# Performance work log

Hardware: AMD Instinct MI355X
Metric: run time of the kernel (lower is better)

## Reference

```python
import jax, jax.numpy as jnp
import numpy as np

NUM_HEADS = 16


def _bayes_w(mu, rho, eps):
    # reparameterized weight sample: w = mu + softplus(rho) * eps
    return mu + jax.nn.softplus(rho) * eps


def setup_inputs() -> dict:
    key = jax.random.key(0)
    ks = jax.random.split(key, 12)
    B, N, C = 4, 2048, 1024
    x = jax.random.normal(ks[0], (B, N, C), jnp.float32)
    w_scale = 0.02
    q_w = jax.random.normal(ks[1], (C, C), jnp.float32) * w_scale
    k_w = jax.random.normal(ks[2], (C, C), jnp.float32) * w_scale
    v_mu = jax.random.normal(ks[3], (C, C), jnp.float32) * w_scale
    v_rho = jax.random.normal(ks[4], (C, C), jnp.float32) * 0.1 - 3.0
    v_eps = jax.random.normal(ks[5], (C, C), jnp.float32)
    proj_mu = jax.random.normal(ks[6], (C, C), jnp.float32) * w_scale
    proj_rho = jax.random.normal(ks[7], (C, C), jnp.float32) * 0.1 - 3.0
    proj_eps = jax.random.normal(ks[8], (C, C), jnp.float32)
    pb_mu = jax.random.normal(ks[9], (C,), jnp.float32) * w_scale
    pb_rho = jax.random.normal(ks[10], (C,), jnp.float32) * 0.1 - 3.0
    pb_eps = jax.random.normal(ks[11], (C,), jnp.float32)
    return {"x": x, "q_w": q_w, "k_w": k_w, "v_mu": v_mu, "v_rho": v_rho,
            "v_eps": v_eps, "proj_mu": proj_mu, "proj_rho": proj_rho,
            "proj_eps": proj_eps, "pb_mu": pb_mu, "pb_rho": pb_rho,
            "pb_eps": pb_eps}


def reference(x, q_w, k_w, v_mu, v_rho, v_eps, proj_mu, proj_rho, proj_eps,
              pb_mu, pb_rho, pb_eps):
    B, N, C = x.shape
    H = NUM_HEADS
    D = C // H
    scale = D ** -0.5
    v_w = _bayes_w(v_mu, v_rho, v_eps)
    # projections (torch Linear: y = x @ W.T)
    q = (x @ q_w.T).reshape(B, N, H, D).transpose(0, 2, 1, 3)  # [B,H,N,D]
    k = (x @ k_w.T).reshape(B, N, H, D).transpose(0, 2, 1, 3)
    v = (x @ v_w.T).reshape(B, N, H, D).transpose(0, 2, 1, 3)
    attn = jax.nn.softmax(jnp.einsum("bhnd,bhmd->bhnm", q * scale, k), axis=-1)
    out = jnp.einsum("bhnm,bhmd->bhnd", attn, v)
    out = out.transpose(0, 2, 1, 3).reshape(B, N, C)
    p_w = _bayes_w(proj_mu, proj_rho, proj_eps)
    p_b = _bayes_w(pb_mu, pb_rho, pb_eps)
    return out @ p_w.T + p_b
```

## Files before the change

### kernel.cpp

```cpp
#include <hip/hip_runtime.h>
#include <hip/hip_bf16.h>
#include <cstdint>
#include <math.h>

typedef __bf16 bf16;
typedef __bf16 bf16x8 __attribute__((ext_vector_type(8)));
typedef __bf16 bf16x4 __attribute__((ext_vector_type(4)));
typedef float  f32x4 __attribute__((ext_vector_type(4)));

#define LOG2E 1.4426950408889634f

#if __has_builtin(__builtin_amdgcn_exp2f)
#define EXP2(x) __builtin_amdgcn_exp2f(x)
#else
#define EXP2(x) exp2f(x)
#endif

#define AS1 __attribute__((address_space(1)))
#define AS3 __attribute__((address_space(3)))

__device__ __forceinline__ void gload_lds16(const bf16* g, bf16* l) {
    __builtin_amdgcn_global_load_lds((AS1 void*)g, (AS3 void*)l, 16, 0, 0);
}

__global__ __launch_bounds__(256)
void cast_f32_bf16(const float* __restrict__ in, bf16* __restrict__ out, int n4) {
    int i = blockIdx.x * 256 + threadIdx.x;
    if (i < n4) {
        float4 v = ((const float4*)in)[i];
        bf16 o[4] = {(bf16)v.x, (bf16)v.y, (bf16)v.z, (bf16)v.w};
        *(uint64_t*)&((bf16*)out)[i * 4] = *(uint64_t*)o;
    }
}

__global__ __launch_bounds__(256)
void bayes_w_kernel(const float* __restrict__ mu, const float* __restrict__ rho,
                    const float* __restrict__ eps, bf16* __restrict__ out, int n) {
    int i = blockIdx.x * 256 + threadIdx.x;
    if (i < n) {
        float r = rho[i];
        float sp = (r > 15.f) ? r : log1pf(expf(r));
        out[i] = (bf16)(mu[i] + sp * eps[i]);
    }
}

__global__ __launch_bounds__(256)
void bayes_b_kernel(const float* __restrict__ mu, const float* __restrict__ rho,
                    const float* __restrict__ eps, float* __restrict__ out, int n) {
    int i = blockIdx.x * 256 + threadIdx.x;
    if (i < n) {
        float r = rho[i];
        float sp = (r > 15.f) ? r : log1pf(expf(r));
        out[i] = mu[i] + sp * eps[i];
    }
}

template <typename OutT>
__global__ __launch_bounds__(256)
void gemm_bt(const bf16* __restrict__ A, const bf16* __restrict__ W,
             OutT* __restrict__ C, const float* __restrict__ bias,
             int M, int N, int K, float q_scale, int q_cols) {
    __shared__ bf16 lA[128 * 32];
    __shared__ bf16 lB[128 * 32];

    const int lane = threadIdx.x & 63;
    const int wv   = threadIdx.x >> 6;
    const int wr   = wv >> 1, wc = wv & 1;
    const int m0 = blockIdx.y * 128, n0 = blockIdx.x * 128;
    const int col = lane & 15, quad = lane >> 4;
    const float scale = (n0 < q_cols) ? q_scale : 1.0f;

    const int srow  = wv * 16 + (lane >> 2);
    const int skcol = (lane & 3) * 8;

    f32x4 acc[4][4] = {};

    for (int k0 = 0; k0 < K; k0 += 32) {
#pragma unroll
        for (int r = 0; r < 2; ++r) {
            gload_lds16(A + (size_t)(m0 + r * 64 + srow) * K + k0 + skcol,
                        &lA[(r * 64 + wv * 16) * 32]);
            gload_lds16(W + (size_t)(n0 + r * 64 + srow) * K + k0 + skcol,
                        &lB[(r * 64 + wv * 16) * 32]);
        }
        __syncthreads();

        bf16x8 af[4], bfr[4];
#pragma unroll
        for (int t = 0; t < 4; ++t) {
            af[t]  = *(const bf16x8*)&lA[(wr * 64 + t * 16 + col) * 32 + quad * 8];
            bfr[t] = *(const bf16x8*)&lB[(wc * 64 + t * 16 + col) * 32 + quad * 8];
        }
#pragma unroll
        for (int i = 0; i < 4; ++i)
#pragma unroll
            for (int j = 0; j < 4; ++j)
                acc[i][j] = __builtin_amdgcn_mfma_f32_16x16x32_bf16(af[i], bfr[j], acc[i][j], 0, 0, 0);
        __syncthreads();
    }

#pragma unroll
    for (int i = 0; i < 4; ++i) {
        int row = m0 + wr * 64 + i * 16 + quad * 4;
#pragma unroll
        for (int j = 0; j < 4; ++j) {
            int cc = n0 + wc * 64 + j * 16 + col;
            float bv = bias ? bias[cc] : 0.f;
#pragma unroll
            for (int r = 0; r < 4; ++r)
                C[(size_t)(row + r) * N + cc] = (OutT)(acc[i][j][r] * scale + bv);
        }
    }
}

__global__ __launch_bounds__(256, 4)
void attn_kernel(const bf16* __restrict__ QKV, bf16* __restrict__ O) {
    __shared__ bf16 sK [64 * 64];
    __shared__ bf16 sVt[64 * 72];
    __shared__ bf16 sP [128 * 72];

    const int lane = threadIdx.x & 63;
    const int wv   = threadIdx.x >> 6;
    const int col  = lane & 15, quad = lane >> 4;
    const int qt = blockIdx.x, h = blockIdx.y, b = blockIdx.z;

    const size_t rowQ0 = (size_t)b * 2048 + qt * 128;
    const bf16* Qg = QKV + rowQ0 * 3072 + h * 64;
    const bf16* Kg = QKV + (size_t)b * 2048 * 3072 + 1024 + h * 64;
    const bf16* Vg = QKV + (size_t)b * 2048 * 3072 + 2048 + h * 64;

#pragma unroll
    for (int it = 0; it < 4; ++it) {
        int c = it * 256 + threadIdx.x;
        int row = c >> 3, dc = (c & 7) * 8;
        *(bf16x8*)&sP[row * 72 + dc] = *(const bf16x8*)&Qg[(size_t)row * 3072 + dc];
    }
    __syncthreads();
    bf16x8 qf[2][2];
#pragma unroll
    for (int mi = 0; mi < 2; ++mi)
#pragma unroll
        for (int ks = 0; ks < 2; ++ks)
            qf[mi][ks] = *(const bf16x8*)&sP[(wv * 32 + mi * 16 + col) * 72 + ks * 32 + quad * 8];

    const int rloc = lane >> 3;
    const bf16* Kdma = Kg + (size_t)(wv * 16 + rloc) * 3072 + (((lane & 7) ^ rloc) * 8);

    f32x4 lsum[2] = {};
    f32x4 o[2][4] = {};
    const int cx = col & 7;

    for (int kv0 = 0; kv0 < 2048; kv0 += 64) {
        gload_lds16(Kdma + (size_t)kv0 * 3072,       &sK[(wv * 16) * 64]);
        gload_lds16(Kdma + (size_t)(kv0 + 8) * 3072, &sK[(wv * 16 + 8) * 64]);
#pragma unroll
        for (int it = 0; it < 2; ++it) {
            int c = it * 256 + threadIdx.x;
            int row = c & 63, dc = (c >> 6) * 8;
            bf16x8 v = *(const bf16x8*)&Vg[(size_t)(kv0 + row) * 3072 + dc];
#pragma unroll
            for (int j = 0; j < 8; ++j) sVt[(dc + j) * 72 + row] = v[j];
        }
        __syncthreads();

        f32x4 st[2][4];
#pragma unroll
        for (int nj = 0; nj < 4; ++nj) {
            bf16x8 kf0 = *(const bf16x8*)&sK[(nj * 16 + col) * 64 + ((quad ^ cx) * 8)];
            bf16x8 kf1 = *(const bf16x8*)&sK[(nj * 16 + col) * 64 + (((quad ^ cx) ^ 4) * 8)];
#pragma unroll
            for (int mi = 0; mi < 2; ++mi) {
                f32x4 t = {0.f, 0.f, 0.f, 0.f};
                t = __builtin_amdgcn_mfma_f32_16x16x32_bf16(kf0, qf[mi][0], t, 0, 0, 0);
                t = __builtin_amdgcn_mfma_f32_16x16x32_bf16(kf1, qf[mi][1], t, 0, 0, 0);
                st[mi][nj] = t;
            }
        }

#pragma unroll
        for (int mi = 0; mi < 2; ++mi) {
#pragma unroll
            for (int nj = 0; nj < 4; ++nj) {
                f32x4 p;
#pragma unroll
                for (int r = 0; r < 4; ++r) p[r] = EXP2(st[mi][nj][r]);
                lsum[mi] += p;
                bf16x4 pk = {(bf16)p[0], (bf16)p[1], (bf16)p[2], (bf16)p[3]};
                *(bf16x4*)&sP[(wv * 32 + mi * 16 + col) * 72 + nj * 16 + quad * 4] = pk;
            }
        }

#pragma unroll
        for (int ks = 0; ks < 2; ++ks) {
            bf16x8 pf0 = *(const bf16x8*)&sP[(wv * 32 + col) * 72 + ks * 32 + quad * 8];
            bf16x8 pf1 = *(const bf16x8*)&sP[(wv * 32 + 16 + col) * 72 + ks * 32 + quad * 8];
#pragma unroll
            for (int dj = 0; dj < 4; ++dj) {
                bf16x8 vf = *(const bf16x8*)&sVt[(dj * 16 + col) * 72 + ks * 32 + quad * 8];
                o[0][dj] = __builtin_amdgcn_mfma_f32_16x16x32_bf16(pf0, vf, o[0][dj], 0, 0, 0);
                o[1][dj] = __builtin_amdgcn_mfma_f32_16x16x32_bf16(pf1, vf, o[1][dj], 0, 0, 0);
            }
        }
        __syncthreads();
    }

#pragma unroll
    for (int mi = 0; mi < 2; ++mi) {
        float l = lsum[mi][0] + lsum[mi][1] + lsum[mi][2] + lsum[mi][3];
        l += __shfl_xor(l, 16, 64);
        l += __shfl_xor(l, 32, 64);
#pragma unroll
        for (int r = 0; r < 4; ++r) {
            float inv = 1.f / __shfl(l, quad * 4 + r, 64);
            size_t row = rowQ0 + wv * 32 + mi * 16 + quad * 4 + r;
#pragma unroll
            for (int dj = 0; dj < 4; ++dj)
                O[row * 1024 + h * 64 + dj * 16 + col] = (bf16)(o[mi][dj][r] * inv);
        }
    }
}

extern "C" void kernel_launch(void* const* d_in, const int* in_sizes, int n_in,
                              void* d_out, int out_size, void* d_ws, size_t ws_size,
                              hipStream_t stream) {
    const float* x      = (const float*)d_in[0];
    const float* q_w    = (const float*)d_in[1];
    const float* k_w    = (const float*)d_in[2];
    const float* v_mu   = (const float*)d_in[3];
    const float* v_rho  = (const float*)d_in[4];
    const float* v_eps  = (const float*)d_in[5];
    const float* p_mu   = (const float*)d_in[6];
    const float* p_rho  = (const float*)d_in[7];
    const float* p_eps  = (const float*)d_in[8];
    const float* pb_mu  = (const float*)d_in[9];
    const float* pb_rho = (const float*)d_in[10];
    const float* pb_eps = (const float*)d_in[11];
    float* out = (float*)d_out;

    const size_t MN = (size_t)8192 * 1024;
    const size_t MB = (size_t)1 << 20;
    char* ws = (char*)d_ws;
    bf16*  xb   = (bf16*)(ws);
    bf16*  wqkv = (bf16*)(ws + 16 * MB);
    bf16*  pwb  = (bf16*)(ws + 22 * MB);
    float* p_b  = (float*)(ws + 24 * MB);
    bf16*  QKV  = (bf16*)(ws + 25 * MB);
    bf16*  Ab   = xb;

    const int Wsz = 1024 * 1024;
    cast_f32_bf16<<<(int)(MN / 4 / 256), 256, 0, stream>>>(x, xb, (int)(MN / 4));
    cast_f32_bf16<<<1024, 256, 0, stream>>>(q_w, wqkv, Wsz / 4);
    cast_f32_bf16<<<1024, 256, 0, stream>>>(k_w, wqkv + Wsz, Wsz / 4);
    bayes_w_kernel<<<4096, 256, 0, stream>>>(v_mu, v_rho, v_eps, wqkv + 2 * Wsz, Wsz);
    bayes_w_kernel<<<4096, 256, 0, stream>>>(p_mu, p_rho, p_eps, pwb, Wsz);
    bayes_b_kernel<<<4, 256, 0, stream>>>(pb_mu, pb_rho, pb_eps, p_b, 1024);

    gemm_bt<bf16><<<dim3(24, 64), 256, 0, stream>>>(xb, wqkv, QKV, nullptr,
                                                    8192, 3072, 1024, 0.125f * LOG2E, 1024);

    attn_kernel<<<dim3(16, 16, 4), 256, 0, stream>>>(QKV, Ab);

    gemm_bt<float><<<dim3(8, 64), 256, 0, stream>>>(Ab, pwb, out, p_b,
                                                    8192, 1024, 1024, 1.0f, 1024);
}
```

Measured before the change: 342.8 us.

## Pre-transpose V, load K/V fragments directly from global, fuse prep kernels

```diff
diff --git a/kernel.cpp b/kernel.cpp
--- a/kernel.cpp
+++ b/kernel.cpp
@@ -7,20 +7,19 @@
 typedef __bf16 bf16x8 __attribute__((ext_vector_type(8)));
 typedef __bf16 bf16x4 __attribute__((ext_vector_type(4)));
 typedef float  f32x4 __attribute__((ext_vector_type(4)));
+typedef unsigned short u16x8 __attribute__((ext_vector_type(8)));
 
 #define LOG2E 1.4426950408889634f
-
-#if __has_builtin(__builtin_amdgcn_exp2f)
-#define EXP2(x) __builtin_amdgcn_exp2f(x)
-#else
-#define EXP2(x) exp2f(x)
-#endif
 
 #define AS1 __attribute__((address_space(1)))
 #define AS3 __attribute__((address_space(3)))
 
 __device__ __forceinline__ void gload_lds16(const bf16* g, bf16* l) {
     __builtin_amdgcn_global_load_lds((AS1 void*)g, (AS3 void*)l, 16, 0, 0);
+}
+
+__device__ __forceinline__ float softplus(float r) {
+    return (r > 15.f) ? r : log1pf(expf(r));
 }
 
 __global__ __launch_bounds__(256)
@@ -29,36 +28,63 @@
     if (i < n4) {
         float4 v = ((const float4*)in)[i];
         bf16 o[4] = {(bf16)v.x, (bf16)v.y, (bf16)v.z, (bf16)v.w};
-        *(uint64_t*)&((bf16*)out)[i * 4] = *(uint64_t*)o;
-    }
-}
-
-__global__ __launch_bounds__(256)
-void bayes_w_kernel(const float* __restrict__ mu, const float* __restrict__ rho,
-                    const float* __restrict__ eps, bf16* __restrict__ out, int n) {
+        *(uint64_t*)&out[i * 4] = *(uint64_t*)o;
+    }
+}
+
+__global__ __launch_bounds__(256)
+void wprep(const float* __restrict__ qw, const float* __restrict__ kw,
+           const float* __restrict__ vmu, const float* __restrict__ vrho,
+           const float* __restrict__ veps, bf16* __restrict__ wqkv) {
     int i = blockIdx.x * 256 + threadIdx.x;
-    if (i < n) {
-        float r = rho[i];
-        float sp = (r > 15.f) ? r : log1pf(expf(r));
-        out[i] = (bf16)(mu[i] + sp * eps[i]);
-    }
-}
-
-__global__ __launch_bounds__(256)
-void bayes_b_kernel(const float* __restrict__ mu, const float* __restrict__ rho,
-                    const float* __restrict__ eps, float* __restrict__ out, int n) {
-    int i = blockIdx.x * 256 + threadIdx.x;
-    if (i < n) {
-        float r = rho[i];
-        float sp = (r > 15.f) ? r : log1pf(expf(r));
-        out[i] = mu[i] + sp * eps[i];
+    int r = blockIdx.y;
+    float4 v;
+    if (r == 0)      v = ((const float4*)qw)[i];
+    else if (r == 1) v = ((const float4*)kw)[i];
+    else {
+        float4 m = ((const float4*)vmu)[i];
+        float4 rh = ((const float4*)vrho)[i];
+        float4 e = ((const float4*)veps)[i];
+        v.x = m.x + softplus(rh.x) * e.x;
+        v.y = m.y + softplus(rh.y) * e.y;
+        v.z = m.z + softplus(rh.z) * e.z;
+        v.w = m.w + softplus(rh.w) * e.w;
+    }
+    bf16 o[4] = {(bf16)v.x, (bf16)v.y, (bf16)v.z, (bf16)v.w};
+    *(uint64_t*)&wqkv[((size_t)r << 20) + (size_t)i * 4] = *(uint64_t*)o;
+}
+
+__global__ __launch_bounds__(256)
+void pprep(const float* __restrict__ pmu, const float* __restrict__ prho,
+           const float* __restrict__ peps, const float* __restrict__ bmu,
+           const float* __restrict__ brho, const float* __restrict__ beps,
+           bf16* __restrict__ pwb, float* __restrict__ p_b) {
+    int bx = blockIdx.x;
+    if (bx < 1024) {
+        int i = bx * 256 + threadIdx.x;
+        float4 m = ((const float4*)pmu)[i];
+        float4 rh = ((const float4*)prho)[i];
+        float4 e = ((const float4*)peps)[i];
+        bf16 o[4] = {(bf16)(m.x + softplus(rh.x) * e.x),
+                     (bf16)(m.y + softplus(rh.y) * e.y),
+                     (bf16)(m.z + softplus(rh.z) * e.z),
+                     (bf16)(m.w + softplus(rh.w) * e.w)};
+        *(uint64_t*)&pwb[(size_t)i * 4] = *(uint64_t*)o;
+    } else {
+        int i = threadIdx.x;
+        float4 m = ((const float4*)bmu)[i];
+        float4 rh = ((const float4*)brho)[i];
+        float4 e = ((const float4*)beps)[i];
+        float4 v = {m.x + softplus(rh.x) * e.x, m.y + softplus(rh.y) * e.y,
+                    m.z + softplus(rh.z) * e.z, m.w + softplus(rh.w) * e.w};
+        ((float4*)p_b)[i] = v;
     }
 }
 
 template <typename OutT>
 __global__ __launch_bounds__(256)
-void gemm_bt(const bf16* __restrict__ A, const bf16* __restrict__ W,
-             OutT* __restrict__ C, const float* __restrict__ bias,
+void gemm_bt(const bf16* __restrict__ A, int lda, const bf16* __restrict__ W,
+             OutT* __restrict__ C, int ldc, const float* __restrict__ bias,
              int M, int N, int K, float q_scale, int q_cols) {
     __shared__ bf16 lA[128 * 32];
     __shared__ bf16 lB[128 * 32];
@@ -78,7 +104,7 @@
     for (int k0 = 0; k0 < K; k0 += 32) {
 #pragma unroll
         for (int r = 0; r < 2; ++r) {
-            gload_lds16(A + (size_t)(m0 + r * 64 + srow) * K + k0 + skcol,
+            gload_lds16(A + (size_t)(m0 + r * 64 + srow) * lda + k0 + skcol,
                         &lA[(r * 64 + wv * 16) * 32]);
             gload_lds16(W + (size_t)(n0 + r * 64 + srow) * K + k0 + skcol,
                         &lB[(r * 64 + wv * 16) * 32]);
@@ -108,16 +134,44 @@
             float bv = bias ? bias[cc] : 0.f;
 #pragma unroll
             for (int r = 0; r < 4; ++r)
-                C[(size_t)(row + r) * N + cc] = (OutT)(acc[i][j][r] * scale + bv);
-        }
-    }
-}
-
-__global__ __launch_bounds__(256, 4)
-void attn_kernel(const bf16* __restrict__ QKV, bf16* __restrict__ O) {
-    __shared__ bf16 sK [64 * 64];
-    __shared__ bf16 sVt[64 * 72];
-    __shared__ bf16 sP [128 * 72];
+                C[(size_t)(row + r) * ldc + cc] = (OutT)(acc[i][j][r] * scale + bv);
+        }
+    }
+}
+
+__global__ __launch_bounds__(256)
+void vtrans(const bf16* __restrict__ QKV, bf16* __restrict__ Vt) {
+    __shared__ uint32_t t[64 * 33];
+    const int tid = threadIdx.x;
+    const int kvt = blockIdx.x, h = blockIdx.y, b = blockIdx.z;
+    const bf16* src = QKV + (size_t)(b * 2048 + kvt * 64) * 3072 + 2048 + h * 64;
+
+    const int kp = tid >> 3, c = tid & 7;
+    u16x8 v0 = *(const u16x8*)&src[(size_t)(2 * kp) * 3072 + c * 8];
+    u16x8 v1 = *(const u16x8*)&src[(size_t)(2 * kp + 1) * 3072 + c * 8];
+#pragma unroll
+    for (int j = 0; j < 8; ++j)
+        t[(c * 8 + j) * 33 + kp] = (uint32_t)v0[j] | ((uint32_t)v1[j] << 16);
+    __syncthreads();
+
+    const int d = tid >> 2, c2 = tid & 3;
+    bf16* dst = &Vt[(size_t)((b * 16 + h) * 64 + d) * 2048 + kvt * 64 + c2 * 16];
+    uint4 w0, w1;
+    w0.x = t[d * 33 + c2 * 8 + 0];
+    w0.y = t[d * 33 + c2 * 8 + 1];
+    w0.z = t[d * 33 + c2 * 8 + 2];
+    w0.w = t[d * 33 + c2 * 8 + 3];
+    w1.x = t[d * 33 + c2 * 8 + 4];
+    w1.y = t[d * 33 + c2 * 8 + 5];
+    w1.z = t[d * 33 + c2 * 8 + 6];
+    w1.w = t[d * 33 + c2 * 8 + 7];
+    *(uint4*)dst       = w0;
+    *(uint4*)(dst + 8) = w1;
+}
+
+__global__ __launch_bounds__(256, 3)
+void attn_kernel(bf16* QKV, const bf16* __restrict__ Vt) {
+    __shared__ bf16 sP[128 * 72];
 
     const int lane = threadIdx.x & 63;
     const int wv   = threadIdx.x >> 6;
@@ -125,9 +179,9 @@
     const int qt = blockIdx.x, h = blockIdx.y, b = blockIdx.z;
 
     const size_t rowQ0 = (size_t)b * 2048 + qt * 128;
-    const bf16* Qg = QKV + rowQ0 * 3072 + h * 64;
+    bf16* Qg = QKV + rowQ0 * 3072 + h * 64;
     const bf16* Kg = QKV + (size_t)b * 2048 * 3072 + 1024 + h * 64;
-    const bf16* Vg = QKV + (size_t)b * 2048 * 3072 + 2048 + h * 64;
+    const bf16* Vg = Vt + (size_t)((b * 16 + h) * 64) * 2048;
 
 #pragma unroll
     for (int it = 0; it < 4; ++it) {
@@ -143,52 +197,44 @@
         for (int ks = 0; ks < 2; ++ks)
             qf[mi][ks] = *(const bf16x8*)&sP[(wv * 32 + mi * 16 + col) * 72 + ks * 32 + quad * 8];
 
-    const int rloc = lane >> 3;
-    const bf16* Kdma = Kg + (size_t)(wv * 16 + rloc) * 3072 + (((lane & 7) ^ rloc) * 8);
-
     f32x4 lsum[2] = {};
     f32x4 o[2][4] = {};
-    const int cx = col & 7;
 
     for (int kv0 = 0; kv0 < 2048; kv0 += 64) {
-        gload_lds16(Kdma + (size_t)kv0 * 3072,       &sK[(wv * 16) * 64]);
-        gload_lds16(Kdma + (size_t)(kv0 + 8) * 3072, &sK[(wv * 16 + 8) * 64]);
-#pragma unroll
-        for (int it = 0; it < 2; ++it) {
-            int c = it * 256 + threadIdx.x;
-            int row = c & 63, dc = (c >> 6) * 8;
-            bf16x8 v = *(const bf16x8*)&Vg[(size_t)(kv0 + row) * 3072 + dc];
-#pragma unroll
-            for (int j = 0; j < 8; ++j) sVt[(dc + j) * 72 + row] = v[j];
-        }
-        __syncthreads();
+        bf16x8 kf[4][2], vf[2][4];
+#pragma unroll
+        for (int nj = 0; nj < 4; ++nj)
+#pragma unroll
+            for (int ks = 0; ks < 2; ++ks)
+                kf[nj][ks] = *(const bf16x8*)&Kg[(size_t)(kv0 + nj * 16 + col) * 3072 + ks * 32 + quad * 8];
+#pragma unroll
+        for (int ks = 0; ks < 2; ++ks)
+#pragma unroll
+            for (int dj = 0; dj < 4; ++dj)
+                vf[ks][dj] = *(const bf16x8*)&Vg[(size_t)(dj * 16 + col) * 2048 + kv0 + ks * 32 + quad * 8];
 
         f32x4 st[2][4];
 #pragma unroll
-        for (int nj = 0; nj < 4; ++nj) {
-            bf16x8 kf0 = *(const bf16x8*)&sK[(nj * 16 + col) * 64 + ((quad ^ cx) * 8)];
-            bf16x8 kf1 = *(const bf16x8*)&sK[(nj * 16 + col) * 64 + (((quad ^ cx) ^ 4) * 8)];
+        for (int nj = 0; nj < 4; ++nj)
 #pragma unroll
             for (int mi = 0; mi < 2; ++mi) {
                 f32x4 t = {0.f, 0.f, 0.f, 0.f};
-                t = __builtin_amdgcn_mfma_f32_16x16x32_bf16(kf0, qf[mi][0], t, 0, 0, 0);
-                t = __builtin_amdgcn_mfma_f32_16x16x32_bf16(kf1, qf[mi][1], t, 0, 0, 0);
+                t = __builtin_amdgcn_mfma_f32_16x16x32_bf16(kf[nj][0], qf[mi][0], t, 0, 0, 0);
+                t = __builtin_amdgcn_mfma_f32_16x16x32_bf16(kf[nj][1], qf[mi][1], t, 0, 0, 0);
                 st[mi][nj] = t;
             }
-        }
-
-#pragma unroll
-        for (int mi = 0; mi < 2; ++mi) {
+
+#pragma unroll
+        for (int mi = 0; mi < 2; ++mi)
 #pragma unroll
             for (int nj = 0; nj < 4; ++nj) {
                 f32x4 p;
 #pragma unroll
-                for (int r = 0; r < 4; ++r) p[r] = EXP2(st[mi][nj][r]);
+                for (int r = 0; r < 4; ++r) p[r] = exp2f(st[mi][nj][r]);
                 lsum[mi] += p;
                 bf16x4 pk = {(bf16)p[0], (bf16)p[1], (bf16)p[2], (bf16)p[3]};
                 *(bf16x4*)&sP[(wv * 32 + mi * 16 + col) * 72 + nj * 16 + quad * 4] = pk;
             }
-        }
 
 #pragma unroll
         for (int ks = 0; ks < 2; ++ks) {
@@ -196,12 +242,10 @@
             bf16x8 pf1 = *(const bf16x8*)&sP[(wv * 32 + 16 + col) * 72 + ks * 32 + quad * 8];
 #pragma unroll
             for (int dj = 0; dj < 4; ++dj) {
-                bf16x8 vf = *(const bf16x8*)&sVt[(dj * 16 + col) * 72 + ks * 32 + quad * 8];
-                o[0][dj] = __builtin_amdgcn_mfma_f32_16x16x32_bf16(pf0, vf, o[0][dj], 0, 0, 0);
-                o[1][dj] = __builtin_amdgcn_mfma_f32_16x16x32_bf16(pf1, vf, o[1][dj], 0, 0, 0);
+                o[0][dj] = __builtin_amdgcn_mfma_f32_16x16x32_bf16(pf0, vf[ks][dj], o[0][dj], 0, 0, 0);
+                o[1][dj] = __builtin_amdgcn_mfma_f32_16x16x32_bf16(pf1, vf[ks][dj], o[1][dj], 0, 0, 0);
             }
         }
-        __syncthreads();
     }
 
 #pragma unroll
@@ -212,10 +256,10 @@
 #pragma unroll
         for (int r = 0; r < 4; ++r) {
             float inv = 1.f / __shfl(l, quad * 4 + r, 64);
-            size_t row = rowQ0 + wv * 32 + mi * 16 + quad * 4 + r;
+            int row = wv * 32 + mi * 16 + quad * 4 + r;
 #pragma unroll
             for (int dj = 0; dj < 4; ++dj)
-                O[row * 1024 + h * 64 + dj * 16 + col] = (bf16)(o[mi][dj][r] * inv);
+                Qg[(size_t)row * 3072 + dj * 16 + col] = (bf16)(o[mi][dj][r] * inv);
         }
     }
 }
@@ -237,7 +281,6 @@
     const float* pb_eps = (const float*)d_in[11];
     float* out = (float*)d_out;
 
-    const size_t MN = (size_t)8192 * 1024;
     const size_t MB = (size_t)1 << 20;
     char* ws = (char*)d_ws;
     bf16*  xb   = (bf16*)(ws);
@@ -245,21 +288,19 @@
     bf16*  pwb  = (bf16*)(ws + 22 * MB);
     float* p_b  = (float*)(ws + 24 * MB);
     bf16*  QKV  = (bf16*)(ws + 25 * MB);
-    bf16*  Ab   = xb;
-
-    const int Wsz = 1024 * 1024;
-    cast_f32_bf16<<<(int)(MN / 4 / 256), 256, 0, stream>>>(x, xb, (int)(MN / 4));
-    cast_f32_bf16<<<1024, 256, 0, stream>>>(q_w, wqkv, Wsz / 4);
-    cast_f32_bf16<<<1024, 256, 0, stream>>>(k_w, wqkv + Wsz, Wsz / 4);
-    bayes_w_kernel<<<4096, 256, 0, stream>>>(v_mu, v_rho, v_eps, wqkv + 2 * Wsz, Wsz);
-    bayes_w_kernel<<<4096, 256, 0, stream>>>(p_mu, p_rho, p_eps, pwb, Wsz);
-    bayes_b_kernel<<<4, 256, 0, stream>>>(pb_mu, pb_rho, pb_eps, p_b, 1024);
-
-    gemm_bt<bf16><<<dim3(24, 64), 256, 0, stream>>>(xb, wqkv, QKV, nullptr,
+    bf16*  Vt   = xb;
+
+    wprep<<<dim3(1024, 3), 256, 0, stream>>>(q_w, k_w, v_mu, v_rho, v_eps, wqkv);
+    pprep<<<1025, 256, 0, stream>>>(p_mu, p_rho, p_eps, pb_mu, pb_rho, pb_eps, pwb, p_b);
+    cast_f32_bf16<<<8192, 256, 0, stream>>>(x, xb, 2097152);
+
+    gemm_bt<bf16><<<dim3(24, 64), 256, 0, stream>>>(xb, 1024, wqkv, QKV, 3072, nullptr,
                                                     8192, 3072, 1024, 0.125f * LOG2E, 1024);
 
-    attn_kernel<<<dim3(16, 16, 4), 256, 0, stream>>>(QKV, Ab);
-
-    gemm_bt<float><<<dim3(8, 64), 256, 0, stream>>>(Ab, pwb, out, p_b,
-                                                    8192, 1024, 1024, 1.0f, 1024);
-}
+    vtrans<<<dim3(32, 16, 4), 256, 0, stream>>>(QKV, Vt);
+
+    attn_kernel<<<dim3(16, 16, 4), 256, 0, stream>>>(QKV, Vt);
+
+    gemm_bt<float><<<dim3(8, 64), 256, 0, stream>>>(QKV, 3072, pwb, out, 1024, p_b,
+                                                    8192, 1024, 1024, 1.0f, 0);
+}
```

Measured after the change: 476.3 us. 1.39x slower.
